# Kernel tuning notes

Hardware: AMD Instinct MI355X
Metric: run time of the kernel (lower is better)

## Reference

```python
import jax, jax.numpy as jnp
import numpy as np

M_A, N_B, S_A, S_B = 2, 2, 1, 1  # sharing chunks and base strides


def setup_inputs() -> dict:
    key = jax.random.key(0)
    ks = jax.random.split(key, 7)
    B, S, D_IN, D_OUT = 4, 2048, 4096, 4096
    U, SHARED_R = 8, 56  # rank=64, unshared u=8
    x = jax.random.normal(ks[0], (B, S, D_IN), jnp.float32)
    W = jax.random.normal(ks[1], (D_OUT, D_IN), jnp.float32) * 0.02
    b = jax.random.normal(ks[2], (D_OUT,), jnp.float32) * 0.02
    A_u = jax.random.normal(ks[3], (U, D_IN), jnp.float32) * 0.02
    B_u = jax.random.normal(ks[4], (D_OUT, U), jnp.float32) * 0.02
    A0_shared = jax.random.normal(ks[5], (SHARED_R, D_IN // M_A), jnp.float32) * 0.02
    B0_shared = jax.random.normal(ks[6], (D_OUT // N_B, SHARED_R), jnp.float32) * 0.02
    return {"x": x, "W": W, "b": b, "A_u": A_u, "B_u": B_u,
            "A0_shared": A0_shared, "B0_shared": B0_shared}


def reference(x, W, b, A_u, B_u, A0_shared, B0_shared):
    # Rotated shared chunks: roll A0 along rank dim (axis 0), tile along in dim.
    A_s = jnp.concatenate([jnp.roll(A0_shared, i * S_A, axis=0) for i in range(M_A)], axis=1)  # [r_s, in]
    # Roll B0 along rank dim (axis 1), tile along out dim.
    B_s = jnp.concatenate([jnp.roll(B0_shared, i * S_B, axis=1) for i in range(N_B)], axis=0)  # [out, r_s]
    # Full delta_W materialization, as in the original module.
    delta_W = B_u @ A_u + B_s @ A_s  # [out, in]
    original = jnp.einsum('bsd,od->bso', x, W) + b
    adapt = jnp.einsum('bsd,od->bso', x, delta_W)
    return original + adapt
```

## Files before the change

kernel.cpp:

```cpp
#include <hip/hip_runtime.h>

typedef unsigned short u16;
typedef __bf16 bf16x8 __attribute__((ext_vector_type(8)));
typedef float f32x4 __attribute__((ext_vector_type(4)));
typedef u16 u16x8 __attribute__((ext_vector_type(8)));

#define M_DIM 8192
#define N_DIM 4096
#define K_DIM 4096
#define BK 64

__device__ __forceinline__ u16 f2b(float f) {
  unsigned int x = __float_as_uint(f);
  unsigned int r = (x + 0x7fffu + ((x >> 16) & 1u)) >> 16;
  return (u16)r;
}

#define GLOAD_LDS16(gp, lp)                                        \
  __builtin_amdgcn_global_load_lds(                                \
      (const __attribute__((address_space(1))) void*)(gp),         \
      (__attribute__((address_space(3))) void*)(lp), 16, 0, 0)

__global__ __launch_bounds__(256) void cvt_x(const float* __restrict__ X,
                                             u16* __restrict__ Xb) {
  const size_t t = (size_t)blockIdx.x * 256 + threadIdx.x;
  const f32x4* src = (const f32x4*)X + t * 2;
  f32x4 a = src[0];
  f32x4 b = src[1];
  u16x8 o;
  o[0] = f2b(a[0]); o[1] = f2b(a[1]); o[2] = f2b(a[2]); o[3] = f2b(a[3]);
  o[4] = f2b(b[0]); o[5] = f2b(b[1]); o[6] = f2b(b[2]); o[7] = f2b(b[3]);
  *((u16x8*)Xb + t) = o;
}

__global__ __launch_bounds__(256) void build_weff(
    const float* __restrict__ W, const float* __restrict__ Au,
    const float* __restrict__ Bu, const float* __restrict__ A0,
    const float* __restrict__ B0, u16* __restrict__ Weff) {
  __shared__ float coef[64 * 16];
  const int t = threadIdx.x;
  const int o0 = blockIdx.y * 16;

#pragma unroll
  for (int j = 0; j < 4; j++) {
    const int idx = t + j * 256;
    const int r = idx >> 4;
    const int oi = idx & 15;
    const int o = o0 + oi;
    float v;
    if (r < 8) {
      v = Bu[o * 8 + r];
    } else {
      const int rs = r - 8;
      if (o < 2048) {
        v = B0[o * 56 + rs];
      } else {
        const int rr = rs ? (rs - 1) : 55;
        v = B0[(o - 2048) * 56 + rr];
      }
    }
    coef[r * 16 + oi] = v;
  }
  __syncthreads();

  const int d0 = blockIdx.x * 1024 + t * 4;
  const int hi = (d0 >= 2048);
  const int dd = hi ? (d0 - 2048) : d0;

  f32x4 acc[16] = {};

#pragma unroll
  for (int r = 0; r < 8; r++) {
    f32x4 a = *(const f32x4*)(Au + (size_t)r * 4096 + d0);
    const float* cr = &coef[r * 16];
#pragma unroll
    for (int oi = 0; oi < 16; oi++) {
      const float c = cr[oi];
      acc[oi][0] += c * a[0]; acc[oi][1] += c * a[1];
      acc[oi][2] += c * a[2]; acc[oi][3] += c * a[3];
    }
  }
#pragma unroll 4
  for (int rs = 0; rs < 56; rs++) {
    const int rr = hi ? (rs ? (rs - 1) : 55) : rs;
    f32x4 a = *(const f32x4*)(A0 + (size_t)rr * 2048 + dd);
    const float* cr = &coef[(rs + 8) * 16];
#pragma unroll
    for (int oi = 0; oi < 16; oi++) {
      const float c = cr[oi];
      acc[oi][0] += c * a[0]; acc[oi][1] += c * a[1];
      acc[oi][2] += c * a[2]; acc[oi][3] += c * a[3];
    }
  }

#pragma unroll
  for (int oi = 0; oi < 16; oi++) {
    f32x4 w = *(const f32x4*)(W + (size_t)(o0 + oi) * 4096 + d0);
    ushort4 ov;
    ov.x = f2b(acc[oi][0] + w[0]);
    ov.y = f2b(acc[oi][1] + w[1]);
    ov.z = f2b(acc[oi][2] + w[2]);
    ov.w = f2b(acc[oi][3] + w[3]);
    *(ushort4*)(Weff + (size_t)(o0 + oi) * 4096 + d0) = ov;
  }
}

__global__ __launch_bounds__(256, 2) void gemm_bt_bias(
    const u16* __restrict__ X, const u16* __restrict__ Wf,
    const float* __restrict__ bias, float* __restrict__ C) {
  __shared__ __align__(16) u16 As[128 * BK];
  __shared__ __align__(16) u16 Bs[128 * BK];

  const int tid = threadIdx.x;
  const int wave = tid >> 6;
  const int lane = tid & 63;
  const int wm = wave >> 1;
  const int wn = wave & 1;
  const int quad = lane >> 4;
  const int l16 = lane & 15;

  const int n0 = blockIdx.x * 128;
  const int m0 = blockIdx.y * 128;

  f32x4 acc[4][4] = {};

  const int srow = lane >> 3;
  const int scb = lane & 7;

  const u16* xg = X + (size_t)(m0 + wave * 32 + srow) * K_DIM + scb * 8;
  const u16* wg = Wf + (size_t)(n0 + wave * 32 + srow) * K_DIM + scb * 8;
  u16* asb = &As[wave * 32 * BK];
  u16* bsb = &Bs[wave * 32 * BK];

  for (int kt = 0; kt < K_DIM; kt += BK) {
#pragma unroll
    for (int q = 0; q < 4; q++) {
      GLOAD_LDS16(xg + (size_t)q * 8 * K_DIM + kt, asb + q * 8 * BK);
      GLOAD_LDS16(wg + (size_t)q * 8 * K_DIM + kt, bsb + q * 8 * BK);
    }
    __syncthreads();

#pragma unroll
    for (int kk = 0; kk < 2; kk++) {
      bf16x8 af[4], bfv[4];
      const int cb = (kk << 2) + quad;
#pragma unroll
      for (int i = 0; i < 4; i++) {
        af[i] = *(const bf16x8*)(&As[(wm * 64 + i * 16 + l16) * BK + cb * 8]);
        bfv[i] = *(const bf16x8*)(&Bs[(wn * 64 + i * 16 + l16) * BK + cb * 8]);
      }
#pragma unroll
      for (int i = 0; i < 4; i++)
#pragma unroll
        for (int j = 0; j < 4; j++)
          acc[i][j] = __builtin_amdgcn_mfma_f32_16x16x32_bf16(
              af[i], bfv[j], acc[i][j], 0, 0, 0);
    }
    __syncthreads();
  }

#pragma unroll
  for (int j = 0; j < 4; j++) {
    const int col = n0 + wn * 64 + j * 16 + l16;
    const float bv = bias[col];
#pragma unroll
    for (int i = 0; i < 4; i++) {
      const int row = m0 + wm * 64 + i * 16 + quad * 4;
#pragma unroll
      for (int r = 0; r < 4; r++) {
        C[(size_t)(row + r) * N_DIM + col] = acc[i][j][r] + bv;
      }
    }
  }
}

extern "C" void kernel_launch(void* const* d_in, const int* in_sizes, int n_in,
                              void* d_out, int out_size, void* d_ws, size_t ws_size,
                              hipStream_t stream) {
  const float* x  = (const float*)d_in[0];
  const float* W  = (const float*)d_in[1];
  const float* b  = (const float*)d_in[2];
  const float* Au = (const float*)d_in[3];
  const float* Bu = (const float*)d_in[4];
  const float* A0 = (const float*)d_in[5];
  const float* B0 = (const float*)d_in[6];
  float* out = (float*)d_out;

  u16* Xb   = (u16*)d_ws;
  u16* Weff = (u16*)((char*)d_ws + (size_t)64 * 1024 * 1024);

  cvt_x<<<16384, 256, 0, stream>>>(x, Xb);
  build_weff<<<dim3(4, 256), 256, 0, stream>>>(W, Au, Bu, A0, B0, Weff);
  gemm_bt_bias<<<dim3(N_DIM / 128, M_DIM / 128), 256, 0, stream>>>(Xb, Weff, b, out);
}
```

Before: 602.0 us.

## Rewrite GEMM with 256x256 tiles, double-buffered LDS pipeline and swizzled layout

The bf16 GEMM moves from 128x128 tiles with 256 threads to 256x256 tiles with 512 threads (8 waves, each owning 128x64). It double-buffers LDS with direct global-to-LDS loads interleaved between four MFMA quarters, using explicit vmcnt waits, barriers and setprio, and XOR-swizzles LDS columns to avoid bank conflicts. A remapped workgroup index groups tiles for cache locality across XCDs. The aim is to hide global load latency and raise MFMA utilisation. In exchange, register pressure goes up and the hand-tuned wait counts have to be exactly right.

```diff
diff --git a/kernel.cpp b/kernel.cpp
--- a/kernel.cpp
+++ b/kernel.cpp
@@ -8,7 +8,10 @@
 #define M_DIM 8192
 #define N_DIM 4096
 #define K_DIM 4096
+#define BM 256
+#define BN 256
 #define BK 64
+#define NT (K_DIM / BK)
 
 __device__ __forceinline__ u16 f2b(float f) {
   unsigned int x = __float_as_uint(f);
@@ -20,6 +23,20 @@
   __builtin_amdgcn_global_load_lds(                                \
       (const __attribute__((address_space(1))) void*)(gp),         \
       (__attribute__((address_space(3))) void*)(lp), 16, 0, 0)
+
+#define SB0 __builtin_amdgcn_sched_barrier(0)
+#define BAR                                                        \
+  do {                                                             \
+    SB0;                                                           \
+    __builtin_amdgcn_s_barrier();                                  \
+    SB0;                                                           \
+  } while (0)
+#define VMW(N)                                                     \
+  do {                                                             \
+    SB0;                                                           \
+    asm volatile("s_waitcnt vmcnt(" #N ")" ::: "memory");          \
+    SB0;                                                           \
+  } while (0)
 
 __global__ __launch_bounds__(256) void cvt_x(const float* __restrict__ X,
                                              u16* __restrict__ Xb) {
@@ -105,67 +122,132 @@
   }
 }
 
-__global__ __launch_bounds__(256, 2) void gemm_bt_bias(
+__global__ __launch_bounds__(512, 2) void gemm_bt_bias(
     const u16* __restrict__ X, const u16* __restrict__ Wf,
     const float* __restrict__ bias, float* __restrict__ C) {
-  __shared__ __align__(16) u16 As[128 * BK];
-  __shared__ __align__(16) u16 Bs[128 * BK];
+  __shared__ __align__(16) u16 lds[65536];
 
   const int tid = threadIdx.x;
   const int wave = tid >> 6;
   const int lane = tid & 63;
-  const int wm = wave >> 1;
-  const int wn = wave & 1;
+  const int wm = wave >> 2;
+  const int wn = wave & 3;
   const int quad = lane >> 4;
   const int l16 = lane & 15;
 
-  const int n0 = blockIdx.x * 128;
-  const int m0 = blockIdx.y * 128;
-
-  f32x4 acc[4][4] = {};
+  const int wgid = ((blockIdx.x & 7) << 6) | (blockIdx.x >> 3);
+  const int n0 = (wgid & 15) * BN;
+  const int m0 = (wgid >> 4) * BM;
 
   const int srow = lane >> 3;
-  const int scb = lane & 7;
-
-  const u16* xg = X + (size_t)(m0 + wave * 32 + srow) * K_DIM + scb * 8;
-  const u16* wg = Wf + (size_t)(n0 + wave * 32 + srow) * K_DIM + scb * 8;
-  u16* asb = &As[wave * 32 * BK];
-  u16* bsb = &Bs[wave * 32 * BK];
-
-  for (int kt = 0; kt < K_DIM; kt += BK) {
-#pragma unroll
-    for (int q = 0; q < 4; q++) {
-      GLOAD_LDS16(xg + (size_t)q * 8 * K_DIM + kt, asb + q * 8 * BK);
-      GLOAD_LDS16(wg + (size_t)q * 8 * K_DIM + kt, bsb + q * 8 * BK);
-    }
-    __syncthreads();
-
-#pragma unroll
-    for (int kk = 0; kk < 2; kk++) {
-      bf16x8 af[4], bfv[4];
-      const int cb = (kk << 2) + quad;
-#pragma unroll
-      for (int i = 0; i < 4; i++) {
-        af[i] = *(const bf16x8*)(&As[(wm * 64 + i * 16 + l16) * BK + cb * 8]);
-        bfv[i] = *(const bf16x8*)(&Bs[(wn * 64 + i * 16 + l16) * BK + cb * 8]);
-      }
-#pragma unroll
-      for (int i = 0; i < 4; i++)
-#pragma unroll
-        for (int j = 0; j < 4; j++)
-          acc[i][j] = __builtin_amdgcn_mfma_f32_16x16x32_bf16(
-              af[i], bfv[j], acc[i][j], 0, 0, 0);
-    }
-    __syncthreads();
-  }
+  const int sq = lane & 7;
+  const int scol = ((sq ^ srow) << 3);
+  const u16* xg = X + (size_t)(m0 + wave * 8 + srow) * K_DIM + scol;
+  const u16* wg = Wf + (size_t)(n0 + wave * 8 + srow) * K_DIM + scol;
+  u16* lA = lds + wave * 512;
+  u16* lB = lds + 32768 + wave * 512;
+
+#define SG_A(b, r, t)                                                       \
+  GLOAD_LDS16(xg + (size_t)(r) * 64 * K_DIM + (size_t)(t) * BK,             \
+              lA + (b) * 16384 + (r) * 4096)
+#define SG_B(b, r, t)                                                       \
+  GLOAD_LDS16(wg + (size_t)(r) * 64 * K_DIM + (size_t)(t) * BK,             \
+              lB + (b) * 16384 + (r) * 4096)
+
+  f32x4 acc[8][4] = {};
+  bf16x8 afr[4][2];
+  bf16x8 bfr[2][2][2];
+
+  const int c0 = (quad << 4) ^ ((l16 & 7) << 4);
+
+#define READ_A(mh)                                                          \
+  do {                                                                      \
+    const char* ab_ = Ab + (size_t)((wm * 128 + (mh) * 64 + l16) * 128);    \
+    _Pragma("unroll") for (int mi = 0; mi < 4; mi++) {                      \
+      afr[mi][0] = *(const bf16x8*)(ab_ + mi * 2048 + c0);                  \
+      afr[mi][1] = *(const bf16x8*)(ab_ + mi * 2048 + (c0 ^ 64));           \
+    }                                                                       \
+  } while (0)
+
+#define READ_B(nh)                                                          \
+  do {                                                                      \
+    const char* bb_ = Bb + (size_t)((wn * 64 + (nh) * 32 + l16) * 128);     \
+    _Pragma("unroll") for (int ni = 0; ni < 2; ni++) {                      \
+      bfr[nh][ni][0] = *(const bf16x8*)(bb_ + ni * 2048 + c0);              \
+      bfr[nh][ni][1] = *(const bf16x8*)(bb_ + ni * 2048 + (c0 ^ 64));       \
+    }                                                                       \
+  } while (0)
+
+#define MFMA_Q(mh, nh)                                                      \
+  do {                                                                      \
+    __builtin_amdgcn_s_setprio(1);                                          \
+    _Pragma("unroll") for (int mi = 0; mi < 4; mi++) {                      \
+      _Pragma("unroll") for (int ni = 0; ni < 2; ni++) {                    \
+        acc[(mh)*4 + mi][(nh)*2 + ni] =                                     \
+            __builtin_amdgcn_mfma_f32_16x16x32_bf16(                        \
+                afr[mi][0], bfr[nh][ni][0],                                 \
+                acc[(mh)*4 + mi][(nh)*2 + ni], 0, 0, 0);                    \
+        acc[(mh)*4 + mi][(nh)*2 + ni] =                                     \
+            __builtin_amdgcn_mfma_f32_16x16x32_bf16(                        \
+                afr[mi][1], bfr[nh][ni][1],                                 \
+                acc[(mh)*4 + mi][(nh)*2 + ni], 0, 0, 0);                    \
+      }                                                                     \
+    }                                                                       \
+    __builtin_amdgcn_s_setprio(0);                                          \
+  } while (0)
+
+  SG_A(0, 0, 0); SG_A(0, 2, 0);
+  SG_B(0, 0, 0); SG_B(0, 1, 0);
+  SG_B(0, 2, 0); SG_B(0, 3, 0);
+  SG_A(0, 1, 0); SG_A(0, 3, 0);
+  SG_A(1, 0, 1); SG_A(1, 2, 1);
+  VMW(4);
+  BAR;
+
+  for (int t = 0; t < NT; ++t) {
+    const int buf = t & 1;
+    const char* Ab = (const char*)lds + buf * 32768;
+    const char* Bb = (const char*)lds + 65536 + buf * 32768;
+    const int t1 = (t + 1 < NT) ? t + 1 : NT - 1;
+    const int t2 = (t + 2 < NT) ? t + 2 : NT - 1;
+    const int b1 = (t + 1) & 1;
+    const int b2 = buf;
+
+    READ_A(0);
+    READ_B(0);
+    SG_B(b1, 0, t1); SG_B(b1, 1, t1);
+    BAR;
+    MFMA_Q(0, 0);
+    BAR;
+
+    READ_B(1);
+    SG_B(b1, 2, t1); SG_B(b1, 3, t1);
+    BAR;
+    MFMA_Q(0, 1);
+    VMW(6);
+    BAR;
+
+    READ_A(1);
+    SG_A(b1, 1, t1); SG_A(b1, 3, t1);
+    BAR;
+    MFMA_Q(1, 1);
+    BAR;
+
+    SG_A(b2, 0, t2); SG_A(b2, 2, t2);
+    BAR;
+    MFMA_Q(1, 0);
+    VMW(4);
+    BAR;
+  }
+  VMW(0);
 
 #pragma unroll
   for (int j = 0; j < 4; j++) {
     const int col = n0 + wn * 64 + j * 16 + l16;
     const float bv = bias[col];
 #pragma unroll
-    for (int i = 0; i < 4; i++) {
-      const int row = m0 + wm * 64 + i * 16 + quad * 4;
+    for (int i = 0; i < 8; i++) {
+      const int row = m0 + wm * 128 + i * 16 + quad * 4;
 #pragma unroll
       for (int r = 0; r < 4; r++) {
         C[(size_t)(row + r) * N_DIM + col] = acc[i][j][r] + bv;
@@ -191,5 +273,5 @@
 
   cvt_x<<<16384, 256, 0, stream>>>(x, Xb);
   build_weff<<<dim3(4, 256), 256, 0, stream>>>(W, Au, Bu, A0, B0, Weff);
-  gemm_bt_bias<<<dim3(N_DIM / 128, M_DIM / 128), 256, 0, stream>>>(Xb, Weff, b, out);
-}
+  gemm_bt_bias<<<dim3(512), dim3(512), 0, stream>>>(Xb, Weff, b, out);
+}
```

Result: faster. 551.9 us (-8.3%).

## Rewrite GEMM with 256x256 tiles, 4-stage LDS pipeline, swizzle and register double-buffering

Applied to the files above, without the earlier changes.

The bf16 GEMM now uses 512-thread blocks computing 256x256 output tiles with BK=32. A four-buffer LDS ring is filled by direct global-to-LDS loads issued three tiles ahead. Fragment reads are double-buffered in registers so MFMA work overlaps the next tile's LDS reads and the global loads. It adds an XOR swizzle against LDS bank conflicts, a remapped block index for L2 locality, and s_setprio around the MFMA bursts. In exchange, register pressure goes up (128 accumulator floats plus two fragment sets per thread) and it relies on hand-placed waitcnt and barriers, which are risky to get right.

```diff
diff --git a/kernel.cpp b/kernel.cpp
--- a/kernel.cpp
+++ b/kernel.cpp
@@ -8,7 +8,10 @@
 #define M_DIM 8192
 #define N_DIM 4096
 #define K_DIM 4096
-#define BK 64
+#define BM 256
+#define BN 256
+#define BK 32
+#define NT (K_DIM / BK)
 
 __device__ __forceinline__ u16 f2b(float f) {
   unsigned int x = __float_as_uint(f);
@@ -20,6 +23,17 @@
   __builtin_amdgcn_global_load_lds(                                \
       (const __attribute__((address_space(1))) void*)(gp),         \
       (__attribute__((address_space(3))) void*)(lp), 16, 0, 0)
+
+#define WAIT8                                                      \
+  do {                                                             \
+    asm volatile("s_waitcnt vmcnt(8) lgkmcnt(0)" ::: "memory");    \
+    __builtin_amdgcn_sched_barrier(0);                             \
+  } while (0)
+#define BARF                                                       \
+  do {                                                             \
+    __builtin_amdgcn_s_barrier();                                  \
+    __builtin_amdgcn_sched_barrier(0);                             \
+  } while (0)
 
 __global__ __launch_bounds__(256) void cvt_x(const float* __restrict__ X,
                                              u16* __restrict__ Xb) {
@@ -105,67 +119,104 @@
   }
 }
 
-__global__ __launch_bounds__(256, 2) void gemm_bt_bias(
+__global__ __launch_bounds__(512, 2) void gemm_bt_bias(
     const u16* __restrict__ X, const u16* __restrict__ Wf,
     const float* __restrict__ bias, float* __restrict__ C) {
-  __shared__ __align__(16) u16 As[128 * BK];
-  __shared__ __align__(16) u16 Bs[128 * BK];
+  __shared__ __align__(16) u16 lds[65536];
 
   const int tid = threadIdx.x;
   const int wave = tid >> 6;
   const int lane = tid & 63;
-  const int wm = wave >> 1;
-  const int wn = wave & 1;
+  const int wm = wave >> 2;
+  const int wn = wave & 3;
   const int quad = lane >> 4;
   const int l16 = lane & 15;
 
-  const int n0 = blockIdx.x * 128;
-  const int m0 = blockIdx.y * 128;
-
-  f32x4 acc[4][4] = {};
-
-  const int srow = lane >> 3;
-  const int scb = lane & 7;
-
-  const u16* xg = X + (size_t)(m0 + wave * 32 + srow) * K_DIM + scb * 8;
-  const u16* wg = Wf + (size_t)(n0 + wave * 32 + srow) * K_DIM + scb * 8;
-  u16* asb = &As[wave * 32 * BK];
-  u16* bsb = &Bs[wave * 32 * BK];
-
-  for (int kt = 0; kt < K_DIM; kt += BK) {
-#pragma unroll
-    for (int q = 0; q < 4; q++) {
-      GLOAD_LDS16(xg + (size_t)q * 8 * K_DIM + kt, asb + q * 8 * BK);
-      GLOAD_LDS16(wg + (size_t)q * 8 * K_DIM + kt, bsb + q * 8 * BK);
-    }
-    __syncthreads();
-
-#pragma unroll
-    for (int kk = 0; kk < 2; kk++) {
-      bf16x8 af[4], bfv[4];
-      const int cb = (kk << 2) + quad;
-#pragma unroll
-      for (int i = 0; i < 4; i++) {
-        af[i] = *(const bf16x8*)(&As[(wm * 64 + i * 16 + l16) * BK + cb * 8]);
-        bfv[i] = *(const bf16x8*)(&Bs[(wn * 64 + i * 16 + l16) * BK + cb * 8]);
-      }
-#pragma unroll
-      for (int i = 0; i < 4; i++)
-#pragma unroll
-        for (int j = 0; j < 4; j++)
-          acc[i][j] = __builtin_amdgcn_mfma_f32_16x16x32_bf16(
-              af[i], bfv[j], acc[i][j], 0, 0, 0);
-    }
-    __syncthreads();
-  }
+  const int wgid = ((blockIdx.x & 7) << 6) | (blockIdx.x >> 3);
+  const int n0 = (wgid & 15) * BN;
+  const int m0 = (wgid >> 4) * BM;
+
+  const int sr = lane >> 2;
+  const int scol = (((lane & 3) ^ ((lane >> 3) & 3)) << 3);
+  const u16* xg = X + (size_t)(m0 + wave * 32 + sr) * K_DIM + scol;
+  const u16* wg = Wf + (size_t)(n0 + wave * 32 + sr) * K_DIM + scol;
+  u16* lA = lds + wave * 1024;
+  u16* lB = lds + 32768 + wave * 1024;
+
+#define SG_A(b, la, kt)                                                     \
+  GLOAD_LDS16(xg + (size_t)(la) * 16 * K_DIM + (size_t)(kt) * BK,           \
+              lA + (b) * 8192 + (la) * 512)
+#define SG_B(b, la, kt)                                                     \
+  GLOAD_LDS16(wg + (size_t)(la) * 16 * K_DIM + (size_t)(kt) * BK,           \
+              lB + (b) * 8192 + (la) * 512)
+#define SG_TILE(b, kt)                                                      \
+  do {                                                                      \
+    SG_A(b, 0, kt); SG_A(b, 1, kt);                                         \
+    SG_B(b, 0, kt); SG_B(b, 1, kt);                                         \
+  } while (0)
+
+  f32x4 acc[8][4] = {};
+  bf16x8 a0[8], b0[4];
+  bf16x8 a1[8], b1[4];
+
+  const int swb = ((quad ^ ((l16 >> 1) & 3)) << 4);
+  const int aoff = (wm * 128 + l16) * 64 + swb;
+  const int boff = 65536 + (wn * 64 + l16) * 64 + swb;
+
+#define READF(AF, BF, b)                                                    \
+  do {                                                                      \
+    const char* p_ = (const char*)lds;                                      \
+    _Pragma("unroll") for (int mi = 0; mi < 8; mi++)                        \
+        AF[mi] = *(const bf16x8*)(p_ + (b) * 16384 + mi * 1024 + aoff);     \
+    _Pragma("unroll") for (int ni = 0; ni < 4; ni++)                        \
+        BF[ni] = *(const bf16x8*)(p_ + (b) * 16384 + ni * 1024 + boff);     \
+  } while (0)
+
+#define MFMA32(AF, BF)                                                      \
+  do {                                                                      \
+    __builtin_amdgcn_s_setprio(1);                                          \
+    _Pragma("unroll") for (int mi = 0; mi < 8; mi++) {                      \
+      _Pragma("unroll") for (int ni = 0; ni < 4; ni++) {                    \
+        acc[mi][ni] = __builtin_amdgcn_mfma_f32_16x16x32_bf16(              \
+            AF[mi], BF[ni], acc[mi][ni], 0, 0, 0);                          \
+      }                                                                     \
+    }                                                                       \
+    __builtin_amdgcn_s_setprio(0);                                          \
+  } while (0)
+
+#define BODY(Tc, SGB, RDB, RA, RB, MA, MB)                                  \
+  do {                                                                      \
+    const int kt_ = ((Tc) + 3 < NT) ? (Tc) + 3 : NT - 1;                    \
+    SG_TILE(SGB, kt_);                                                      \
+    WAIT8;                                                                  \
+    BARF;                                                                   \
+    READF(RA, RB, RDB);                                                     \
+    MFMA32(MA, MB);                                                         \
+  } while (0)
+
+  SG_TILE(0, 0);
+  SG_TILE(1, 1);
+  SG_TILE(2, 2);
+  WAIT8;
+  BARF;
+  READF(a0, b0, 0);
+
+  for (int u = 0; u < NT / 4; ++u) {
+    const int T = u * 4;
+    BODY(T + 0, 3, 1, a1, b1, a0, b0);
+    BODY(T + 1, 0, 2, a0, b0, a1, b1);
+    BODY(T + 2, 1, 3, a1, b1, a0, b0);
+    BODY(T + 3, 2, 0, a0, b0, a1, b1);
+  }
+  asm volatile("s_waitcnt vmcnt(0)" ::: "memory");
 
 #pragma unroll
   for (int j = 0; j < 4; j++) {
     const int col = n0 + wn * 64 + j * 16 + l16;
     const float bv = bias[col];
 #pragma unroll
-    for (int i = 0; i < 4; i++) {
-      const int row = m0 + wm * 64 + i * 16 + quad * 4;
+    for (int i = 0; i < 8; i++) {
+      const int row = m0 + wm * 128 + i * 16 + quad * 4;
 #pragma unroll
       for (int r = 0; r < 4; r++) {
         C[(size_t)(row + r) * N_DIM + col] = acc[i][j][r] + bv;
@@ -191,5 +242,5 @@
 
   cvt_x<<<16384, 256, 0, stream>>>(x, Xb);
   build_weff<<<dim3(4, 256), 256, 0, stream>>>(W, Au, Bu, A0, B0, Weff);
-  gemm_bt_bias<<<dim3(N_DIM / 128, M_DIM / 128), 256, 0, stream>>>(Xb, Weff, b, out);
-}
+  gemm_bt_bias<<<dim3(512), dim3(512), 0, stream>>>(Xb, Weff, b, out);
+}
```

Result: slower. 614.9 us (+2.1%).
